# Kernel optimization log

Hardware: AMD Instinct MI355X
Metric: run time of the kernel (lower is better)

## Reference

```python
import jax, jax.numpy as jnp
import numpy as np

N, E = 25000, 400000
NF, EF, HNF, HEF = 32, 32, 128, 128
NOUT, EOUT = 32, 32
D_N, D_E = HNF + NF, HEF + EF  # concat dims fed to the GNN layer


def _glorot(key, shape):
    return jax.random.normal(key, shape, jnp.float32) / np.sqrt(shape[0])


def setup_inputs() -> dict:
    key = jax.random.key(0)
    ks = jax.random.split(key, 10)
    return {
        "nf": jax.random.normal(ks[0], (N, NF), jnp.float32),
        "ef": jax.random.normal(ks[1], (E, EF), jnp.float32),
        "src": jax.random.randint(ks[2], (E,), 0, N),
        "dst": jax.random.randint(ks[3], (E,), 0, N),
        # AttnMPNNLayer params: edge model, attention logit model, node model
        "W_edge": _glorot(ks[4], (2 * D_N + D_E, HEF)),
        "b_edge": jnp.zeros((HEF,), jnp.float32),
        "W_attn": _glorot(ks[5], (2 * D_N + D_E, 1)),
        "b_attn": jnp.zeros((1,), jnp.float32),
        "W_node": _glorot(ks[6], (D_N + HEF, HNF)),
        "b_node": jnp.zeros((HNF,), jnp.float32),
        # output heads (MLP with num_neurons=[] -> single Linear)
        "W_nout": _glorot(ks[7], (HNF, NOUT)),
        "b_nout": jnp.zeros((NOUT,), jnp.float32),
        "W_eout": _glorot(ks[8], (HEF, EOUT)),
        "b_eout": jnp.zeros((EOUT,), jnp.float32),
        "n_iters": 3,
    }


def _attn_mpnn_layer(hnf, hef, src, dst, W_edge, b_edge, W_attn, b_attn, W_node, b_node):
    """Attention message passing: gather endpoints, edge MLP + attn logit,
    edge-softmax over incoming edges (per dst node), scatter-aggregate, node MLP."""
    n = hnf.shape[0]
    e_in = jnp.concatenate([hnf[src], hnf[dst], hef], axis=-1)   # [E, 2*D_N + D_E]
    m = jax.nn.relu(e_in @ W_edge + b_edge)                      # [E, HEF] new edge feats
    logit = (e_in @ W_attn + b_attn)[:, 0]                       # [E]
    # numerically stable edge softmax grouped by destination node
    lmax = jax.ops.segment_max(logit, dst, num_segments=n)
    lmax = jnp.where(jnp.isfinite(lmax), lmax, 0.0)              # isolated nodes -> 0
    a = jnp.exp(logit - lmax[dst])
    denom = jax.ops.segment_sum(a, dst, num_segments=n)
    alpha = a / jnp.maximum(denom[dst], 1e-16)
    agg = jax.ops.segment_sum(alpha[:, None] * m, dst, num_segments=n)  # [N, HEF]
    un = jax.nn.relu(jnp.concatenate([hnf, agg], axis=-1) @ W_node + b_node)  # [N, HNF]
    return un, m


def reference(nf, ef, src, dst, W_edge, b_edge, W_attn, b_attn, W_node, b_node,
              W_nout, b_nout, W_eout, b_eout, n_iters):
    hnf = jnp.zeros((nf.shape[0], HNF), nf.dtype)
    hef = jnp.zeros((ef.shape[0], HEF), ef.dtype)
    for _ in range(n_iters):
        hnf = jnp.concatenate([hnf, nf], axis=-1)   # input re-injection
        hef = jnp.concatenate([hef, ef], axis=-1)
        hnf, hef = _attn_mpnn_layer(hnf, hef, src, dst,
                                    W_edge, b_edge, W_attn, b_attn, W_node, b_node)
    unf = hnf @ W_nout + b_nout
    uef = hef @ W_eout + b_eout
    return unf, uef
```

## Files before the change

kernel.cpp:

```cpp
#include <hip/hip_runtime.h>


#define GN 25000
#define GE 400000
#define NODE_BLKS 196
#define EDGE_BLKS 6250
#define HEAD_EBLKS 3125

typedef unsigned short u16;
typedef __attribute__((ext_vector_type(8))) short bf16x8;
typedef __attribute__((ext_vector_type(4))) float f32x4;

__device__ inline float b2f(u16 v) {
  union { unsigned int u; float f; } x; x.u = ((unsigned int)v) << 16; return x.f;
}
__device__ inline u16 f2b(float f) {
  union { float f; unsigned int u; } x; x.f = f;
  unsigned int u = x.u;
  u += 0x7fffu + ((u >> 16) & 1u);
  return (u16)(u >> 16);
}

__global__ void detect_dtype(const void* nf, int* flag) {
  if (blockIdx.x == 0 && threadIdx.x == 0) {
    const u16* p = (const u16*)nf;
    int cnt = 0;
    for (int i = 0; i < 512; i += 2) {
      int e = (p[i] >> 7) & 0xFF;
      if (e >= 0x70 && e <= 0x85) cnt++;
    }
    *flag = (cnt < 128) ? 1 : 0;
  }
}

__global__ void convert_kernel(const void* src, u16* dst, long n, const int* flag) {
  int f32 = *flag;
  long i = (long)blockIdx.x * blockDim.x + threadIdx.x;
  long stride = (long)gridDim.x * blockDim.x;
  for (; i < n; i += stride)
    dst[i] = f32 ? f2b(((const float*)src)[i]) : ((const u16*)src)[i];
}

__global__ void gather_ef(const void* ef, const int* eid, u16* efc, const int* flag) {
  int f32 = *flag;
  long idx = (long)blockIdx.x * blockDim.x + threadIdx.x;
  long stride = (long)gridDim.x * blockDim.x;
  long ntot = (long)GE * 32;
  for (; idx < ntot; idx += stride) {
    long j = idx >> 5;
    int c = (int)(idx & 31);
    long e = eid[j];
    efc[idx] = f32 ? f2b(((const float*)ef)[e * 32 + c]) : ((const u16*)ef)[e * 32 + c];
  }
}

__global__ void prep_weights(const void* We, const void* Wn, const void* Wa,
                             const void* Won, const void* Woe,
                             const void* be, const void* ba, const void* bn,
                             const void* bno, const void* beo,
                             u16* WeT, u16* WnpT, u16* WnuT, u16* WoN, u16* WoE,
                             u16* Wac, u16* bec, u16* bac, u16* bnc, u16* bnoc, u16* beoc,
                             const int* flag) {
  int f32 = *flag;
  auto ld = [&](const void* p, long i) -> u16 {
    return f32 ? f2b(((const float*)p)[i]) : ((const u16*)p)[i];
  };
  int tid = blockIdx.x * blockDim.x + threadIdx.x;
  int nt = gridDim.x * blockDim.x;
  for (int i = tid; i < 128 * 160; i += nt) { int n = i / 160, k = i % 160; WeT[i] = ld(We, (long)(320 + k) * 128 + n); }
  for (int i = tid; i < 256 * 160; i += nt) {
    int c = i / 160, k = i % 160;
    WnpT[i] = (c < 128) ? ld(We, (long)k * 128 + c) : ld(We, (long)(160 + k) * 128 + (c - 128));
  }
  for (int i = tid; i < 128 * 288; i += nt) { int c = i / 288, k = i % 288; WnuT[i] = ld(Wn, (long)k * 128 + c); }
  for (int i = tid; i < 32 * 128; i += nt) {
    int c = i / 128, k = i % 128;
    WoN[i] = ld(Won, (long)k * 32 + c);
    WoE[i] = ld(Woe, (long)k * 32 + c);
  }
  for (int i = tid; i < 480; i += nt) Wac[i] = ld(Wa, i);
  for (int i = tid; i < 128; i += nt) { bec[i] = ld(be, i); bnc[i] = ld(bn, i); }
  for (int i = tid; i < 32; i += nt) { bnoc[i] = ld(bno, i); beoc[i] = ld(beo, i); }
  if (tid == 0) bac[0] = ld(ba, 0);
}

__global__ void hist_kernel(const int* dst, int* counts, int n) {
  for (int e = blockIdx.x * blockDim.x + threadIdx.x; e < n; e += gridDim.x * blockDim.x)
    atomicAdd(&counts[dst[e]], 1);
}

__global__ __launch_bounds__(256) void scan_kernel(int* cursor, int* rowptr, int n) {
  __shared__ int part[256];
  int t = threadIdx.x;
  int per = (n + 255) / 256;
  int lo = t * per;
  int hi = lo + per; if (hi > n) hi = n;
  if (lo > n) lo = n;
  int s = 0;
  for (int i = lo; i < hi; ++i) s += cursor[i];
  part[t] = s;
  __syncthreads();
  for (int off = 1; off < 256; off <<= 1) {
    int v = (t >= off) ? part[t - off] : 0;
    __syncthreads();
    part[t] += v;
    __syncthreads();
  }
  int run = (t > 0) ? part[t - 1] : 0;
  for (int i = lo; i < hi; ++i) {
    int c = cursor[i];
    cursor[i] = run;
    rowptr[i + 1] = run + c;
    run += c;
  }
  if (t == 0) rowptr[0] = 0;
}

__global__ void fill_kernel(const int* src, const int* dst, int* cursor, int* eid,
                            int* srcs, int* dsts, int n) {
  for (int e = blockIdx.x * blockDim.x + threadIdx.x; e < n; e += gridDim.x * blockDim.x) {
    int d = dst[e];
    int p = atomicAdd(&cursor[d], 1);
    eid[p] = e;
    srcs[p] = src[e];
    dsts[p] = d;
  }
}

__global__ __launch_bounds__(256)
void node_proj(const u16* HNF, const u16* nf, const u16* WnpT, const u16* W_attn,
               u16* Xs, u16* Xd, float* as_, float* ad_, int kc0, int nrows) {
  __shared__ union {
    struct { __align__(16) u16 A[128][40]; __align__(16) u16 B[128][40]; } st;
    u16 C[128][130];
  } sm;
  __shared__ float dotbuf[128][2];
  int sel = blockIdx.y, blk = blockIdx.x, tid = threadIdx.x;
  int lane = tid & 63, wv = tid >> 6, wr = wv & 1, wc = wv >> 1;
  const u16* BT = WnpT + sel * 128 * 160;
  u16* OUT = sel ? Xd : Xs;
  float* AOUT = sel ? ad_ : as_;
  const u16* wa = W_attn + sel * 160;
  f32x4 acc[4][4];
  f32x4 zf = {0.f, 0.f, 0.f, 0.f};
  for (int i = 0; i < 4; ++i) for (int j = 0; j < 4; ++j) acc[i][j] = zf;
  float dp = 0.f;
  int arow = tid >> 1, ahalf = (tid & 1) * 16;
  int r0 = blk * 128;
  for (int kc = kc0; kc < 5; ++kc) {
    {
      int r = r0 + arow;
      uint4 v0 = make_uint4(0, 0, 0, 0), v1 = make_uint4(0, 0, 0, 0);
      if (r < nrows) {
        const uint4* p = (kc < 4) ? (const uint4*)(HNF + (size_t)r * 128 + kc * 32 + ahalf)
                                  : (const uint4*)(nf + (size_t)r * 32 + ahalf);
        v0 = p[0]; v1 = p[1];
      }
      *(uint4*)&sm.st.A[arow][ahalf] = v0;
      *(uint4*)&sm.st.A[arow][ahalf + 8] = v1;
    }
    {
      const uint4* p = (const uint4*)(BT + arow * 160 + kc * 32 + ahalf);
      uint4 v0 = p[0], v1 = p[1];
      *(uint4*)&sm.st.B[arow][ahalf] = v0;
      *(uint4*)&sm.st.B[arow][ahalf + 8] = v1;
    }
    __syncthreads();
    {
      float s = 0.f;
      for (int j = 0; j < 16; ++j) s += b2f(sm.st.A[arow][ahalf + j]) * b2f(wa[kc * 32 + ahalf + j]);
      dp += s;
    }
    int q = lane >> 4, l16 = lane & 15;
    bf16x8 af[4], bfr[4];
    for (int i = 0; i < 4; ++i) af[i] = *(const bf16x8*)&sm.st.A[wr * 64 + i * 16 + l16][q * 8];
    for (int j = 0; j < 4; ++j) bfr[j] = *(const bf16x8*)&sm.st.B[wc * 64 + j * 16 + l16][q * 8];
    for (int i = 0; i < 4; ++i)
      for (int j = 0; j < 4; ++j)
        acc[i][j] = __builtin_amdgcn_mfma_f32_16x16x32_bf16(af[i], bfr[j], acc[i][j], 0, 0, 0);
    __syncthreads();
  }
  dotbuf[arow][tid & 1] = dp;
  {
    int q = lane >> 4, l16 = lane & 15;
    for (int i = 0; i < 4; ++i)
      for (int j = 0; j < 4; ++j) {
        int col = wc * 64 + j * 16 + l16;
        for (int rr = 0; rr < 4; ++rr) {
          int row = wr * 64 + i * 16 + q * 4 + rr;
          sm.C[row][col] = f2b(acc[i][j][rr]);
        }
      }
  }
  __syncthreads();
  if (tid < 128) {
    int r = r0 + tid;
    if (r < nrows) AOUT[r] = dotbuf[tid][0] + dotbuf[tid][1];
  }
  {
    int r = tid >> 1, h = (tid & 1) * 64;
    int rg = r0 + r;
    if (rg < nrows) {
      uint4* po = (uint4*)(OUT + (size_t)rg * 128 + h);
      for (int k = 0; k < 8; ++k) {
        unsigned int a0 = *(const unsigned int*)&sm.C[r][h + k * 8];
        unsigned int a1 = *(const unsigned int*)&sm.C[r][h + k * 8 + 2];
        unsigned int a2 = *(const unsigned int*)&sm.C[r][h + k * 8 + 4];
        unsigned int a3 = *(const unsigned int*)&sm.C[r][h + k * 8 + 6];
        po[k] = make_uint4(a0, a1, a2, a3);
      }
    }
  }
}

template <int KC0>
__global__ __launch_bounds__(256, 4)
void edge_fused(u16* HEF, const u16* ef, const u16* WeT, const u16* W_attn,
                const u16* b_edge, const u16* b_attn, const int* srcs, const int* dsts,
                const u16* Xs, const u16* Xd, const float* as_, const float* ad_,
                float* logit) {
  __shared__ union {
    __align__(16) u16 A[2][64][40];
    float C[64][65];
  } sm;
  __shared__ float dotbuf[64];
  int blk = blockIdx.x, tid = threadIdx.x;
  int lane = tid & 63, wv = tid >> 6, wr = wv & 1, wc = wv >> 1;
  int q = lane >> 4, l16 = lane & 15;
  f32x4 acc[2][4];
  f32x4 zf = {0.f, 0.f, 0.f, 0.f};
  for (int i = 0; i < 2; ++i) for (int j = 0; j < 4; ++j) acc[i][j] = zf;
  float dp[2] = {0.f, 0.f};
  long e0 = (long)blk * 64;
  long ea = e0 + (tid >> 2);
  int qp = (tid & 3) * 8;
  const u16* wa = W_attn + 320;

  uint4 va = (KC0 < 4) ? *(const uint4*)(HEF + ea * 128 + KC0 * 32 + qp)
                       : *(const uint4*)(ef + ea * 32 + qp);
  bf16x8 bfp[2][4];
#pragma unroll
  for (int j = 0; j < 4; ++j)
    bfp[KC0 & 1][j] = *(const bf16x8*)(WeT + (size_t)(wc * 64 + j * 16 + l16) * 160 + KC0 * 32 + q * 8);

#pragma unroll
  for (int kc = KC0; kc < 5; ++kc) {
    int buf = kc & 1;
    *(uint4*)&sm.A[buf][tid >> 2][qp] = va;
    if (kc < 4) {
      va = (kc + 1 < 4) ? *(const uint4*)(HEF + ea * 128 + (kc + 1) * 32 + qp)
                        : *(const uint4*)(ef + ea * 32 + qp);
#pragma unroll
      for (int j = 0; j < 4; ++j)
        bfp[(kc + 1) & 1][j] = *(const bf16x8*)(WeT + (size_t)(wc * 64 + j * 16 + l16) * 160 + (kc + 1) * 32 + q * 8);
    }
    __syncthreads();
    bf16x8 af[2];
    for (int i = 0; i < 2; ++i) af[i] = *(const bf16x8*)&sm.A[buf][wr * 32 + i * 16 + l16][q * 8];
    if (wc == 0) {
      bf16x8 wv8 = *(const bf16x8*)&wa[kc * 32 + q * 8];
      float wf[8];
      for (int j = 0; j < 8; ++j) wf[j] = b2f((u16)wv8[j]);
      for (int i = 0; i < 2; ++i)
        for (int j = 0; j < 8; ++j) dp[i] += b2f((u16)af[i][j]) * wf[j];
    }
    for (int i = 0; i < 2; ++i)
      for (int j = 0; j < 4; ++j)
        acc[i][j] = __builtin_amdgcn_mfma_f32_16x16x32_bf16(af[i], bfp[buf][j], acc[i][j], 0, 0, 0);
  }
  if (wc == 0) {
    for (int i = 0; i < 2; ++i) {
      dp[i] += __shfl_xor(dp[i], 16);
      dp[i] += __shfl_xor(dp[i], 32);
    }
    if (q == 0)
      for (int i = 0; i < 2; ++i) dotbuf[wr * 32 + i * 16 + l16] = dp[i];
  }
  int r = tid >> 2, qh = tid & 3;
  long e = e0 + r;
  int s = srcs[e], d = dsts[e];
#pragma unroll
  for (int p = 0; p < 2; ++p) {
    int cb = p * 64 + qh * 16;
    const uint4* ps = (const uint4*)(Xs + (size_t)s * 128 + cb);
    const uint4* pd = (const uint4*)(Xd + (size_t)d * 128 + cb);
    uint4 gs0 = ps[0], gs1 = ps[1], gd0 = pd[0], gd1 = pd[1];
    __syncthreads();
    if (wc == p) {
      for (int i = 0; i < 2; ++i)
        for (int j = 0; j < 4; ++j) {
          int col = j * 16 + l16;
          float bb = b2f(b_edge[p * 64 + col]);
          for (int rr = 0; rr < 4; ++rr)
            sm.C[wr * 32 + i * 16 + q * 4 + rr][col] = acc[i][j][rr] + bb;
        }
    }
    __syncthreads();
    if (p == 0 && tid < 64) {
      long ee = e0 + tid;
      logit[ee] = dotbuf[tid] + as_[srcs[ee]] + ad_[dsts[ee]] + b2f(b_attn[0]);
    }
    unsigned int us[8], ud[8];
    *(uint4*)&us[0] = gs0; *(uint4*)&us[4] = gs1;
    *(uint4*)&ud[0] = gd0; *(uint4*)&ud[4] = gd1;
    unsigned int ov[8];
    for (int w = 0; w < 8; ++w) {
      float c0 = sm.C[r][qh * 16 + 2 * w];
      float c1 = sm.C[r][qh * 16 + 2 * w + 1];
      float v0 = c0 + b2f((u16)(us[w] & 0xffffu)) + b2f((u16)(ud[w] & 0xffffu));
      float v1 = c1 + b2f((u16)(us[w] >> 16)) + b2f((u16)(ud[w] >> 16));
      ov[w] = (unsigned int)f2b(fmaxf(v0, 0.f)) | ((unsigned int)f2b(fmaxf(v1, 0.f)) << 16);
    }
    uint4* po = (uint4*)(HEF + e * 128 + cb);
    po[0] = *(uint4*)&ov[0];
    po[1] = *(uint4*)&ov[4];
  }
}

__global__ __launch_bounds__(256)
void aggregate(const int* rowptr, const float* logit, const u16* M, u16* AGG, int nrows) {
  int gw = (blockIdx.x * blockDim.x + threadIdx.x) >> 6;
  int lane = threadIdx.x & 63;
  if (gw >= nrows) return;
  int beg = rowptr[gw], end = rowptr[gw + 1];
  int sub = lane >> 3, cl = lane & 7;
  float mx = -1e30f;
  for (int j = beg + lane; j < end; j += 64) mx = fmaxf(mx, logit[j]);
  for (int off = 32; off > 0; off >>= 1) mx = fmaxf(mx, __shfl_xor(mx, off));
  float acc[16];
  for (int t = 0; t < 16; ++t) acc[t] = 0.f;
  float denom = 0.f;
  for (int j0 = beg; j0 < end; j0 += 8) {
    int j = j0 + sub;
    float w = 0.f;
    uint4 m0 = make_uint4(0, 0, 0, 0), m1 = make_uint4(0, 0, 0, 0);
    if (j < end) {
      w = __expf(logit[j] - mx);
      const uint4* mp = (const uint4*)(M + (size_t)j * 128 + cl * 16);
      m0 = mp[0]; m1 = mp[1];
    }
    denom += w;
    const unsigned int* mw0 = (const unsigned int*)&m0;
    const unsigned int* mw1 = (const unsigned int*)&m1;
    for (int t = 0; t < 4; ++t) {
      acc[2 * t]     += w * b2f((u16)(mw0[t] & 0xffffu));
      acc[2 * t + 1] += w * b2f((u16)(mw0[t] >> 16));
      acc[8 + 2 * t]     += w * b2f((u16)(mw1[t] & 0xffffu));
      acc[8 + 2 * t + 1] += w * b2f((u16)(mw1[t] >> 16));
    }
  }
  denom += __shfl_xor(denom, 8);
  denom += __shfl_xor(denom, 16);
  denom += __shfl_xor(denom, 32);
  for (int t = 0; t < 16; ++t) {
    acc[t] += __shfl_xor(acc[t], 8);
    acc[t] += __shfl_xor(acc[t], 16);
    acc[t] += __shfl_xor(acc[t], 32);
  }
  float inv = 1.0f / fmaxf(denom, 1e-16f);
  if (sub == 0) {
    unsigned int ov[8];
    for (int t = 0; t < 8; ++t)
      ov[t] = (unsigned int)f2b(acc[2 * t] * inv) | ((unsigned int)f2b(acc[2 * t + 1] * inv) << 16);
    uint4* po = (uint4*)(AGG + (size_t)gw * 128 + cl * 16);
    po[0] = *(uint4*)&ov[0];
    po[1] = *(uint4*)&ov[4];
  }
}

__global__ __launch_bounds__(256)
void node_update(u16* HNF, const u16* nf, const u16* AGG, const u16* WnuT,
                 const u16* b_node, int kc0, int nrows) {
  __shared__ union {
    struct { __align__(16) u16 A[128][40]; __align__(16) u16 B[128][40]; } st;
    u16 C[128][130];
  } sm;
  int blk = blockIdx.x, tid = threadIdx.x;
  int lane = tid & 63, wv = tid >> 6, wr = wv & 1, wc = wv >> 1;
  f32x4 acc[4][4];
  f32x4 zf = {0.f, 0.f, 0.f, 0.f};
  for (int i = 0; i < 4; ++i) for (int j = 0; j < 4; ++j) acc[i][j] = zf;
  int arow = tid >> 1, ahalf = (tid & 1) * 16;
  int r0 = blk * 128;
  for (int kc = kc0; kc < 9; ++kc) {
    {
      int r = r0 + arow;
      uint4 v0 = make_uint4(0, 0, 0, 0), v1 = make_uint4(0, 0, 0, 0);
      if (r < nrows) {
        const u16* p;
        if (kc < 4) p = HNF + (size_t)r * 128 + kc * 32 + ahalf;
        else if (kc == 4) p = nf + (size_t)r * 32 + ahalf;
        else p = AGG + (size_t)r * 128 + (kc - 5) * 32 + ahalf;
        v0 = ((const uint4*)p)[0];
        v1 = ((const uint4*)p)[1];
      }
      *(uint4*)&sm.st.A[arow][ahalf] = v0;
      *(uint4*)&sm.st.A[arow][ahalf + 8] = v1;
    }
    {
      const uint4* p = (const uint4*)(WnuT + arow * 288 + kc * 32 + ahalf);
      uint4 v0 = p[0], v1 = p[1];
      *(uint4*)&sm.st.B[arow][ahalf] = v0;
      *(uint4*)&sm.st.B[arow][ahalf + 8] = v1;
    }
    __syncthreads();
    int q = lane >> 4, l16 = lane & 15;
    bf16x8 af[4], bfr[4];
    for (int i = 0; i < 4; ++i) af[i] = *(const bf16x8*)&sm.st.A[wr * 64 + i * 16 + l16][q * 8];
    for (int j = 0; j < 4; ++j) bfr[j] = *(const bf16x8*)&sm.st.B[wc * 64 + j * 16 + l16][q * 8];
    for (int i = 0; i < 4; ++i)
      for (int j = 0; j < 4; ++j)
        acc[i][j] = __builtin_amdgcn_mfma_f32_16x16x32_bf16(af[i], bfr[j], acc[i][j], 0, 0, 0);
    __syncthreads();
  }
  int q = lane >> 4, l16 = lane & 15;
  for (int i = 0; i < 4; ++i)
    for (int j = 0; j < 4; ++j) {
      int col = wc * 64 + j * 16 + l16;
      float bb = b2f(b_node[col]);
      for (int rr = 0; rr < 4; ++rr) {
        int row = wr * 64 + i * 16 + q * 4 + rr;
        sm.C[row][col] = f2b(fmaxf(acc[i][j][rr] + bb, 0.f));
      }
    }
  __syncthreads();
  {
    int r = tid >> 1, h = (tid & 1) * 64;
    int rg = r0 + r;
    if (rg < nrows) {
      uint4* po = (uint4*)(HNF + (size_t)rg * 128 + h);
      for (int k = 0; k < 8; ++k) {
        unsigned int a0 = *(const unsigned int*)&sm.C[r][h + k * 8];
        unsigned int a1 = *(const unsigned int*)&sm.C[r][h + k * 8 + 2];
        unsigned int a2 = *(const unsigned int*)&sm.C[r][h + k * 8 + 4];
        unsigned int a3 = *(const unsigned int*)&sm.C[r][h + k * 8 + 6];
        po[k] = make_uint4(a0, a1, a2, a3);
      }
    }
  }
}

__global__ __launch_bounds__(256)
void head_kernel(const u16* IN, const u16* WT, const u16* bias, float* OUT, long R,
                 const int* remap) {
  __shared__ __align__(16) u16 Asm[128][40];
  __shared__ __align__(16) u16 Bsm[32][40];
  int blk = blockIdx.x, tid = threadIdx.x;
  int lane = tid & 63, wv = tid >> 6;
  f32x4 acc[2][2];
  f32x4 zf = {0.f, 0.f, 0.f, 0.f};
  for (int i = 0; i < 2; ++i) for (int j = 0; j < 2; ++j) acc[i][j] = zf;
  int arow = tid >> 1, ahalf = (tid & 1) * 16;
  long r0 = (long)blk * 128;
  for (int kc = 0; kc < 4; ++kc) {
    {
      long r = r0 + arow;
      uint4 v0 = make_uint4(0, 0, 0, 0), v1 = make_uint4(0, 0, 0, 0);
      if (r < R) {
        const uint4* p = (const uint4*)(IN + r * 128 + kc * 32 + ahalf);
        v0 = p[0]; v1 = p[1];
      }
      *(uint4*)&Asm[arow][ahalf] = v0;
      *(uint4*)&Asm[arow][ahalf + 8] = v1;
    }
    if (tid < 64) {
      const uint4* p = (const uint4*)(WT + arow * 128 + kc * 32 + ahalf);
      uint4 v0 = p[0], v1 = p[1];
      *(uint4*)&Bsm[arow][ahalf] = v0;
      *(uint4*)&Bsm[arow][ahalf + 8] = v1;
    }
    __syncthreads();
    int q = lane >> 4, l16 = lane & 15;
    bf16x8 af[2], bfr[2];
    for (int i = 0; i < 2; ++i) af[i] = *(const bf16x8*)&Asm[wv * 32 + i * 16 + l16][q * 8];
    for (int j = 0; j < 2; ++j) bfr[j] = *(const bf16x8*)&Bsm[j * 16 + l16][q * 8];
    for (int i = 0; i < 2; ++i)
      for (int j = 0; j < 2; ++j)
        acc[i][j] = __builtin_amdgcn_mfma_f32_16x16x32_bf16(af[i], bfr[j], acc[i][j], 0, 0, 0);
    __syncthreads();
  }
  int q = lane >> 4, l16 = lane & 15;
  for (int i = 0; i < 2; ++i)
    for (int rr = 0; rr < 4; ++rr) {
      long r = r0 + wv * 32 + i * 16 + q * 4 + rr;
      if (r < R) {
        long ro = remap ? (long)remap[r] : r;
        for (int j = 0; j < 2; ++j) {
          int col = j * 16 + l16;
          OUT[ro * 32 + col] = acc[i][j][rr] + b2f(bias[col]);
        }
      }
    }
}

extern "C" void kernel_launch(void* const* d_in, const int* in_sizes, int n_in,
                              void* d_out, int out_size, void* d_ws, size_t ws_size,
                              hipStream_t stream) {
  const size_t REQUIRED = 160000000;
  if (ws_size < REQUIRED) return;

  const void* nf_r = d_in[0];
  const void* ef_r = d_in[1];
  const int* src = (const int*)d_in[2];
  const int* dst = (const int*)d_in[3];

  char* ws = (char*)d_ws;
  auto alloc = [&](size_t bytes) {
    char* p = ws;
    ws += (bytes + 255) & ~(size_t)255;
    return p;
  };
  u16* HEF = (u16*)alloc((size_t)GE * 128 * 2);
  u16* HNF = (u16*)alloc((size_t)GN * 128 * 2);
  u16* Xs = (u16*)alloc((size_t)GN * 128 * 2);
  u16* Xd = (u16*)alloc((size_t)GN * 128 * 2);
  float* as_ = (float*)alloc((size_t)GN * 4);
  float* ad_ = (float*)alloc((size_t)GN * 4);
  float* logit = (float*)alloc((size_t)GE * 4);
  int* rowptr = (int*)alloc((size_t)(GN + 1) * 4);
  int* cursor = (int*)alloc((size_t)GN * 4);
  int* eid = (int*)alloc((size_t)GE * 4);
  int* srcs = (int*)alloc((size_t)GE * 4);
  int* dsts = (int*)alloc((size_t)GE * 4);
  u16* WeT = (u16*)alloc(128 * 160 * 2);
  u16* WnpT = (u16*)alloc(256 * 160 * 2);
  u16* WnuT = (u16*)alloc(128 * 288 * 2);
  u16* WoN = (u16*)alloc(32 * 128 * 2);
  u16* WoE = (u16*)alloc(32 * 128 * 2);
  u16* nfc = (u16*)alloc((size_t)GN * 32 * 2);
  u16* efc = (u16*)alloc((size_t)GE * 32 * 2);
  u16* bec = (u16*)alloc(128 * 2);
  u16* Wac = (u16*)alloc(480 * 2);
  u16* bac = (u16*)alloc(2);
  u16* bnc = (u16*)alloc(128 * 2);
  u16* bnoc = (u16*)alloc(32 * 2);
  u16* beoc = (u16*)alloc(32 * 2);
  int* dflag = (int*)alloc(4);
  u16* AGG = Xs;

  detect_dtype<<<1, 64, 0, stream>>>(nf_r, dflag);
  hipMemsetAsync(cursor, 0, (size_t)GN * 4, stream);
  hist_kernel<<<1563, 256, 0, stream>>>(dst, cursor, GE);
  scan_kernel<<<1, 256, 0, stream>>>(cursor, rowptr, GN);
  fill_kernel<<<1563, 256, 0, stream>>>(src, dst, cursor, eid, srcs, dsts, GE);

  convert_kernel<<<784, 256, 0, stream>>>(nf_r, nfc, (long)GN * 32, dflag);
  gather_ef<<<6250, 256, 0, stream>>>(ef_r, eid, efc, dflag);
  prep_weights<<<128, 256, 0, stream>>>(d_in[4], d_in[8], d_in[6], d_in[10], d_in[12],
                                        d_in[5], d_in[7], d_in[9], d_in[11], d_in[13],
                                        WeT, WnpT, WnuT, WoN, WoE,
                                        Wac, bec, bac, bnc, bnoc, beoc, dflag);

  for (int iter = 0; iter < 3; ++iter) {
    int kc0 = (iter == 0) ? 4 : 0;
    dim3 npgrid(NODE_BLKS, 2);
    node_proj<<<npgrid, 256, 0, stream>>>(HNF, nfc, WnpT, Wac, Xs, Xd, as_, ad_, kc0, GN);
    if (iter == 0)
      edge_fused<4><<<EDGE_BLKS, 256, 0, stream>>>(HEF, efc, WeT, Wac, bec, bac, srcs, dsts,
                                                   Xs, Xd, as_, ad_, logit);
    else
      edge_fused<0><<<EDGE_BLKS, 256, 0, stream>>>(HEF, efc, WeT, Wac, bec, bac, srcs, dsts,
                                                   Xs, Xd, as_, ad_, logit);
    aggregate<<<(GN + 3) / 4, 256, 0, stream>>>(rowptr, logit, HEF, AGG, GN);
    node_update<<<NODE_BLKS, 256, 0, stream>>>(HNF, nfc, AGG, WnuT, bnc, kc0, GN);
  }

  float* out_nf = (float*)d_out;
  float* out_ef = (float*)d_out + (size_t)GN * 32;
  head_kernel<<<NODE_BLKS, 256, 0, stream>>>(HNF, WoN, bnoc, out_nf, GN, nullptr);
  head_kernel<<<HEAD_EBLKS, 256, 0, stream>>>(HEF, WoE, beoc, out_ef, GE, eid);
}
```

Measured before the change: 655.8 us.

## Vectorize ef gather, widen scan, load edge A-fragments directly, prefetch aggregate

gather_ef now handles 8 columns per thread with 16-byte loads and stores instead of scalar element copies. The single-block scan uses 1024 threads to shorten each thread's serial portion. edge_fused loads A fragments straight from global memory into registers with double buffering, dropping the LDS staging and the per-step barrier but creating more uncoalesced, redundant global loads. aggregate software-pipelines the next edge's weight and message loads to hide latency, at the cost of more registers.

```diff
diff --git a/kernel.cpp b/kernel.cpp
--- a/kernel.cpp
+++ b/kernel.cpp
@@ -44,14 +44,25 @@
 __global__ void gather_ef(const void* ef, const int* eid, u16* efc, const int* flag) {
   int f32 = *flag;
   long idx = (long)blockIdx.x * blockDim.x + threadIdx.x;
-  long stride = (long)gridDim.x * blockDim.x;
-  long ntot = (long)GE * 32;
-  for (; idx < ntot; idx += stride) {
-    long j = idx >> 5;
-    int c = (int)(idx & 31);
-    long e = eid[j];
-    efc[idx] = f32 ? f2b(((const float*)ef)[e * 32 + c]) : ((const u16*)ef)[e * 32 + c];
-  }
+  long ntot = (long)GE * 4;
+  if (idx >= ntot) return;
+  long j = idx >> 2;
+  int g = (int)(idx & 3) * 8;
+  long e = eid[j];
+  uint4 out;
+  if (f32) {
+    const float* pf = (const float*)ef + e * 32 + g;
+    float4 a = ((const float4*)pf)[0];
+    float4 b = ((const float4*)pf)[1];
+    unsigned int* ov = (unsigned int*)&out;
+    ov[0] = (unsigned int)f2b(a.x) | ((unsigned int)f2b(a.y) << 16);
+    ov[1] = (unsigned int)f2b(a.z) | ((unsigned int)f2b(a.w) << 16);
+    ov[2] = (unsigned int)f2b(b.x) | ((unsigned int)f2b(b.y) << 16);
+    ov[3] = (unsigned int)f2b(b.z) | ((unsigned int)f2b(b.w) << 16);
+  } else {
+    out = *(const uint4*)((const u16*)ef + e * 32 + g);
+  }
+  *(uint4*)(efc + j * 32 + g) = out;
 }
 
 __global__ void prep_weights(const void* We, const void* Wn, const void* Wa,
@@ -89,10 +100,10 @@
     atomicAdd(&counts[dst[e]], 1);
 }
 
-__global__ __launch_bounds__(256) void scan_kernel(int* cursor, int* rowptr, int n) {
-  __shared__ int part[256];
+__global__ __launch_bounds__(1024) void scan_kernel(int* cursor, int* rowptr, int n) {
+  __shared__ int part[1024];
   int t = threadIdx.x;
-  int per = (n + 255) / 256;
+  int per = (n + 1023) / 1024;
   int lo = t * per;
   int hi = lo + per; if (hi > n) hi = n;
   if (lo > n) lo = n;
@@ -100,7 +111,7 @@
   for (int i = lo; i < hi; ++i) s += cursor[i];
   part[t] = s;
   __syncthreads();
-  for (int off = 1; off < 256; off <<= 1) {
+  for (int off = 1; off < 1024; off <<= 1) {
     int v = (t >= off) ? part[t - off] : 0;
     __syncthreads();
     part[t] += v;
@@ -219,10 +230,7 @@
                 const u16* b_edge, const u16* b_attn, const int* srcs, const int* dsts,
                 const u16* Xs, const u16* Xd, const float* as_, const float* ad_,
                 float* logit) {
-  __shared__ union {
-    __align__(16) u16 A[2][64][40];
-    float C[64][65];
-  } sm;
+  __shared__ float C[64][65];
   __shared__ float dotbuf[64];
   int blk = blockIdx.x, tid = threadIdx.x;
   int lane = tid & 63, wv = tid >> 6, wr = wv & 1, wc = wv >> 1;
@@ -232,41 +240,42 @@
   for (int i = 0; i < 2; ++i) for (int j = 0; j < 4; ++j) acc[i][j] = zf;
   float dp[2] = {0.f, 0.f};
   long e0 = (long)blk * 64;
-  long ea = e0 + (tid >> 2);
-  int qp = (tid & 3) * 8;
   const u16* wa = W_attn + 320;
-
-  uint4 va = (KC0 < 4) ? *(const uint4*)(HEF + ea * 128 + KC0 * 32 + qp)
-                       : *(const uint4*)(ef + ea * 32 + qp);
-  bf16x8 bfp[2][4];
+  long ar = e0 + wr * 32 + l16;
+  const u16* aH0 = HEF + ar * 128 + q * 8;
+  const u16* aH1 = aH0 + 16 * 128;
+  const u16* aE0 = ef + ar * 32 + q * 8;
+  const u16* aE1 = aE0 + 16 * 32;
+  const u16* bW = WeT + (size_t)(wc * 64 + l16) * 160 + q * 8;
+
+  bf16x8 afp[2][2], bfp[2][4];
 #pragma unroll
   for (int j = 0; j < 4; ++j)
-    bfp[KC0 & 1][j] = *(const bf16x8*)(WeT + (size_t)(wc * 64 + j * 16 + l16) * 160 + KC0 * 32 + q * 8);
+    bfp[KC0 & 1][j] = *(const bf16x8*)(bW + (size_t)j * 16 * 160 + KC0 * 32);
+  afp[KC0 & 1][0] = (KC0 < 4) ? *(const bf16x8*)(aH0 + KC0 * 32) : *(const bf16x8*)aE0;
+  afp[KC0 & 1][1] = (KC0 < 4) ? *(const bf16x8*)(aH1 + KC0 * 32) : *(const bf16x8*)aE1;
 
 #pragma unroll
   for (int kc = KC0; kc < 5; ++kc) {
-    int buf = kc & 1;
-    *(uint4*)&sm.A[buf][tid >> 2][qp] = va;
+    int cur = kc & 1, nxt = cur ^ 1;
     if (kc < 4) {
-      va = (kc + 1 < 4) ? *(const uint4*)(HEF + ea * 128 + (kc + 1) * 32 + qp)
-                        : *(const uint4*)(ef + ea * 32 + qp);
+      int kn = kc + 1;
+      afp[nxt][0] = (kn < 4) ? *(const bf16x8*)(aH0 + kn * 32) : *(const bf16x8*)aE0;
+      afp[nxt][1] = (kn < 4) ? *(const bf16x8*)(aH1 + kn * 32) : *(const bf16x8*)aE1;
 #pragma unroll
       for (int j = 0; j < 4; ++j)
-        bfp[(kc + 1) & 1][j] = *(const bf16x8*)(WeT + (size_t)(wc * 64 + j * 16 + l16) * 160 + (kc + 1) * 32 + q * 8);
-    }
-    __syncthreads();
-    bf16x8 af[2];
-    for (int i = 0; i < 2; ++i) af[i] = *(const bf16x8*)&sm.A[buf][wr * 32 + i * 16 + l16][q * 8];
+        bfp[nxt][j] = *(const bf16x8*)(bW + (size_t)j * 16 * 160 + kn * 32);
+    }
     if (wc == 0) {
       bf16x8 wv8 = *(const bf16x8*)&wa[kc * 32 + q * 8];
       float wf[8];
       for (int j = 0; j < 8; ++j) wf[j] = b2f((u16)wv8[j]);
       for (int i = 0; i < 2; ++i)
-        for (int j = 0; j < 8; ++j) dp[i] += b2f((u16)af[i][j]) * wf[j];
+        for (int j = 0; j < 8; ++j) dp[i] += b2f((u16)afp[cur][i][j]) * wf[j];
     }
     for (int i = 0; i < 2; ++i)
       for (int j = 0; j < 4; ++j)
-        acc[i][j] = __builtin_amdgcn_mfma_f32_16x16x32_bf16(af[i], bfp[buf][j], acc[i][j], 0, 0, 0);
+        acc[i][j] = __builtin_amdgcn_mfma_f32_16x16x32_bf16(afp[cur][i], bfp[cur][j], acc[i][j], 0, 0, 0);
   }
   if (wc == 0) {
     for (int i = 0; i < 2; ++i) {
@@ -292,7 +301,7 @@
           int col = j * 16 + l16;
           float bb = b2f(b_edge[p * 64 + col]);
           for (int rr = 0; rr < 4; ++rr)
-            sm.C[wr * 32 + i * 16 + q * 4 + rr][col] = acc[i][j][rr] + bb;
+            C[wr * 32 + i * 16 + q * 4 + rr][col] = acc[i][j][rr] + bb;
         }
     }
     __syncthreads();
@@ -305,8 +314,8 @@
     *(uint4*)&ud[0] = gd0; *(uint4*)&ud[4] = gd1;
     unsigned int ov[8];
     for (int w = 0; w < 8; ++w) {
-      float c0 = sm.C[r][qh * 16 + 2 * w];
-      float c1 = sm.C[r][qh * 16 + 2 * w + 1];
+      float c0 = C[r][qh * 16 + 2 * w];
+      float c1 = C[r][qh * 16 + 2 * w + 1];
       float v0 = c0 + b2f((u16)(us[w] & 0xffffu)) + b2f((u16)(ud[w] & 0xffffu));
       float v1 = c1 + b2f((u16)(us[w] >> 16)) + b2f((u16)(ud[w] >> 16));
       ov[w] = (unsigned int)f2b(fmaxf(v0, 0.f)) | ((unsigned int)f2b(fmaxf(v1, 0.f)) << 16);
@@ -330,24 +339,35 @@
   float acc[16];
   for (int t = 0; t < 16; ++t) acc[t] = 0.f;
   float denom = 0.f;
+  float wc = 0.f;
+  uint4 m0c = make_uint4(0, 0, 0, 0), m1c = make_uint4(0, 0, 0, 0);
+  {
+    int j = beg + sub;
+    if (j < end) {
+      wc = __expf(logit[j] - mx);
+      const uint4* mp = (const uint4*)(M + (size_t)j * 128 + cl * 16);
+      m0c = mp[0]; m1c = mp[1];
+    }
+  }
   for (int j0 = beg; j0 < end; j0 += 8) {
-    int j = j0 + sub;
-    float w = 0.f;
-    uint4 m0 = make_uint4(0, 0, 0, 0), m1 = make_uint4(0, 0, 0, 0);
-    if (j < end) {
-      w = __expf(logit[j] - mx);
-      const uint4* mp = (const uint4*)(M + (size_t)j * 128 + cl * 16);
-      m0 = mp[0]; m1 = mp[1];
-    }
-    denom += w;
-    const unsigned int* mw0 = (const unsigned int*)&m0;
-    const unsigned int* mw1 = (const unsigned int*)&m1;
+    float wn = 0.f;
+    uint4 m0n = make_uint4(0, 0, 0, 0), m1n = make_uint4(0, 0, 0, 0);
+    int jn = j0 + 8 + sub;
+    if (jn < end) {
+      wn = __expf(logit[jn] - mx);
+      const uint4* mp = (const uint4*)(M + (size_t)jn * 128 + cl * 16);
+      m0n = mp[0]; m1n = mp[1];
+    }
+    denom += wc;
+    const unsigned int* mw0 = (const unsigned int*)&m0c;
+    const unsigned int* mw1 = (const unsigned int*)&m1c;
     for (int t = 0; t < 4; ++t) {
-      acc[2 * t]     += w * b2f((u16)(mw0[t] & 0xffffu));
-      acc[2 * t + 1] += w * b2f((u16)(mw0[t] >> 16));
-      acc[8 + 2 * t]     += w * b2f((u16)(mw1[t] & 0xffffu));
-      acc[8 + 2 * t + 1] += w * b2f((u16)(mw1[t] >> 16));
-    }
+      acc[2 * t]     += wc * b2f((u16)(mw0[t] & 0xffffu));
+      acc[2 * t + 1] += wc * b2f((u16)(mw0[t] >> 16));
+      acc[8 + 2 * t]     += wc * b2f((u16)(mw1[t] & 0xffffu));
+      acc[8 + 2 * t + 1] += wc * b2f((u16)(mw1[t] >> 16));
+    }
+    wc = wn; m0c = m0n; m1c = m1n;
   }
   denom += __shfl_xor(denom, 8);
   denom += __shfl_xor(denom, 16);
@@ -541,7 +561,7 @@
   detect_dtype<<<1, 64, 0, stream>>>(nf_r, dflag);
   hipMemsetAsync(cursor, 0, (size_t)GN * 4, stream);
   hist_kernel<<<1563, 256, 0, stream>>>(dst, cursor, GE);
-  scan_kernel<<<1, 256, 0, stream>>>(cursor, rowptr, GN);
+  scan_kernel<<<1, 1024, 0, stream>>>(cursor, rowptr, GN);
   fill_kernel<<<1563, 256, 0, stream>>>(src, dst, cursor, eid, srcs, dsts, GE);
 
   convert_kernel<<<784, 256, 0, stream>>>(nf_r, nfc, (long)GN * 32, dflag);
```

Result: no change. 648.1 us (-1.2%).
